# Kernel tuning notes

Measured on AMD Instinct MI355X. Metric: run time of the kernel, lower is better.

Reference implementation:

```python
import jax, jax.numpy as jnp
import numpy as np

NC = 80          # classes
REG_MAX = 16     # DFL bins
NK = 51          # 17*3 keypoint channels
KPT_SHAPE = (17, 3)
MAX_DET = 100
CONF_THRES = 0.25
STRIDES = (8, 16, 32)


def _conv1x1(f, w, b):
    # f: (B,C,H,W), w: (O,C), b: (O,) -> (B,O,H,W)
    return jnp.einsum('bchw,oc->bohw', f, w) + b[None, :, None, None]


def _make_anchors(shapes, strides, offset=0.5):
    pts, sts = [], []
    for (h, w), s in zip(shapes, strides):
        sx = jnp.arange(w, dtype=jnp.float32) + offset
        sy = jnp.arange(h, dtype=jnp.float32) + offset
        gy, gx = jnp.meshgrid(sy, sx, indexing='ij')
        pts.append(jnp.stack([gx, gy], -1).reshape(-1, 2))
        sts.append(jnp.full((h * w, 1), float(s), jnp.float32))
    # transposed as in _new_inference: anchors (2,A), strides (1,A)
    return jnp.concatenate(pts, 0).T, jnp.concatenate(sts, 0).T


def setup_inputs() -> dict:
    key = jax.random.key(0)
    ks = jax.random.split(key, 16)
    ch = (128, 256, 512)
    hw = ((80, 80), (40, 40), (20, 20))
    d = {}
    for i, (c, (h, w)) in enumerate(zip(ch, hw)):
        d[f'x{i}'] = jax.random.normal(ks[i], (16, c, h, w), jnp.float32)
    k = 3
    for name, oc in (('cv2', 4 * REG_MAX), ('cv3', NC), ('cv4', NK)):
        for i, c in enumerate(ch):
            d[f'{name}_w{i}'] = jax.random.normal(ks[k], (oc, c), jnp.float32) * 0.02
            d[f'{name}_b{i}'] = jnp.zeros((oc,), jnp.float32)
            k += 1
    return d


def reference(x0, x1, x2,
              cv2_w0, cv2_b0, cv2_w1, cv2_b1, cv2_w2, cv2_b2,
              cv3_w0, cv3_b0, cv3_w1, cv3_b1, cv3_w2, cv3_b2,
              cv4_w0, cv4_b0, cv4_w1, cv4_b1, cv4_w2, cv4_b2):
    feats = [x0, x1, x2]
    cv2 = [(cv2_w0, cv2_b0), (cv2_w1, cv2_b1), (cv2_w2, cv2_b2)]
    cv3 = [(cv3_w0, cv3_b0), (cv3_w1, cv3_b1), (cv3_w2, cv3_b2)]
    cv4 = [(cv4_w0, cv4_b0), (cv4_w1, cv4_b1), (cv4_w2, cv4_b2)]
    bs = x0.shape[0]

    # keypoint branch: cat over levels -> (bs, nk, A)
    kpt = jnp.concatenate(
        [_conv1x1(f, w, b).reshape(bs, NK, -1) for f, (w, b) in zip(feats, cv4)], -1)
    # box+cls branch -> (bs, 4*reg_max+nc, A)
    xcat = jnp.concatenate(
        [jnp.concatenate([_conv1x1(f, *cv2[i]), _conv1x1(f, *cv3[i])], 1).reshape(bs, 4 * REG_MAX + NC, -1)
         for i, f in enumerate(feats)], -1)
    box, cls = xcat[:, :4 * REG_MAX], xcat[:, 4 * REG_MAX:]

    shapes = [(f.shape[2], f.shape[3]) for f in feats]
    anchors, strides = _make_anchors(shapes, STRIDES)  # (2,A), (1,A)
    A = anchors.shape[1]

    # DFL decode: softmax over reg_max bins, expectation w/ arange weights
    p = jax.nn.softmax(box.reshape(bs, 4, REG_MAX, A), axis=2)
    dist = jnp.einsum('bfra,r->bfa', p, jnp.arange(REG_MAX, dtype=jnp.float32))
    lt, rb = dist[:, :2], dist[:, 2:]
    x1y1 = anchors[None] - lt
    x2y2 = anchors[None] + rb
    # xywh box coding, scaled by strides
    dbox = jnp.concatenate([(x1y1 + x2y2) * 0.5, x2y2 - x1y1], 1) * strides[None]  # (bs,4,A)

    # keypoint decode (Pose.kpts_decode, ndim==3)
    y = kpt.reshape(bs, KPT_SHAPE[0], KPT_SHAPE[1], A)
    kxy = (y[:, :, :2] * 2.0 + (anchors[None, None] - 0.5)) * strides[None, None]
    kv = jax.nn.sigmoid(y[:, :, 2:3])
    pred_kpts = jnp.concatenate([kxy, kv], 2).reshape(bs, NK, A).transpose(0, 2, 1)  # (bs,A,nk)

    # EfficientIdxNMS_TRT stand-in: sigmoid scores (score_activation=1),
    # class-agnostic deterministic top-k selection by best class score.
    scores = jax.nn.sigmoid(cls.transpose(0, 2, 1))  # (bs,A,nc)
    max_s = scores.max(-1)
    cls_id = jnp.argmax(scores, -1)
    top_s, top_i = jax.lax.top_k(max_s, MAX_DET)     # (bs,MAX_DET)
    num_dets = (top_s > CONF_THRES).sum(-1).astype(jnp.int32)[:, None]
    det_boxes = jnp.take_along_axis(dbox.transpose(0, 2, 1), top_i[..., None], 1)  # (bs,MAX_DET,4)
    det_classes = jnp.take_along_axis(cls_id, top_i, 1).astype(jnp.int32)
    # irregular keypoint gather via det indices (the pred_kpts[bs_indices, det_indices] step)
    det_kpts = jnp.take_along_axis(pred_kpts, top_i[..., None], 1).reshape(bs, MAX_DET, *KPT_SHAPE)
    return num_dets, det_boxes, top_s, det_classes, det_kpts
```

## Files before the change

### kernel.cpp

```cpp
#include <hip/hip_runtime.h>
#include <hip/hip_bf16.h>

#define NC 80
#define NK 51
#define REG_MAX 16
#define MAX_DET 100
#define A_TOT 8400
#define BS 16

#define OUT_NUM 0
#define OUT_BOX 16
#define OUT_SCORE (16 + 16*MAX_DET*4)
#define OUT_CLASS (OUT_SCORE + 16*MAX_DET)
#define OUT_KPT (OUT_CLASS + 16*MAX_DET)

static __device__ __forceinline__ unsigned long long mk_key(unsigned u, int a) {
    return ((unsigned long long)u << 32) | (unsigned)(0x7FFFFFFF - a);
}

template<int C, int A>
static __device__ __forceinline__ void score_tile(
    const float* __restrict__ x, const float* __restrict__ w,
    const float* __restrict__ bias,
    int b, int a0, int a_off,
    float* __restrict__ max_s, int* __restrict__ cls_id,
    float* __restrict__ wsh, float (*rm)[256], int (*ri)[256])
{
    int t = threadIdx.x;
    int lane = t & 63;
    int wv = t >> 6;
    int oc0 = wv * 10;

    int aa = a0 + lane * 4;
    if (aa > A - 4) aa = A - 4;
    const float* xb = x + (long)b * C * A + aa;

    float acc[10][4];
#pragma unroll
    for (int j = 0; j < 10; ++j) {
        float bv = bias[oc0 + j];
        acc[j][0] = bv; acc[j][1] = bv; acc[j][2] = bv; acc[j][3] = bv;
    }

    int nchunk = C >> 5;
    for (int kc = 0; kc < nchunk; ++kc) {
        int cbase = kc * 32;
        if (kc) __syncthreads();
#pragma unroll
        for (int i = 0; i < 2; ++i) {
            int idx = t + i * 512;
            if (idx < 640) {
                int oc = idx >> 3;
                int q = idx & 7;
                float4 v = *(const float4*)(w + oc * C + cbase + q * 4);
                *(float4*)(&wsh[idx * 4]) = v;
            }
        }
        __syncthreads();

#pragma unroll 2
        for (int c4 = 0; c4 < 32; c4 += 4) {
            const float* fp = xb + (long)(cbase + c4) * A;
            float4 f0 = *(const float4*)(fp);
            float4 f1 = *(const float4*)(fp + A);
            float4 f2 = *(const float4*)(fp + 2 * A);
            float4 f3 = *(const float4*)(fp + 3 * A);
#pragma unroll
            for (int j = 0; j < 10; ++j) {
                float4 w4 = *(const float4*)(&wsh[(oc0 + j) * 32 + c4]);
                acc[j][0] = fmaf(w4.x, f0.x, acc[j][0]);
                acc[j][0] = fmaf(w4.y, f1.x, acc[j][0]);
                acc[j][0] = fmaf(w4.z, f2.x, acc[j][0]);
                acc[j][0] = fmaf(w4.w, f3.x, acc[j][0]);
                acc[j][1] = fmaf(w4.x, f0.y, acc[j][1]);
                acc[j][1] = fmaf(w4.y, f1.y, acc[j][1]);
                acc[j][1] = fmaf(w4.z, f2.y, acc[j][1]);
                acc[j][1] = fmaf(w4.w, f3.y, acc[j][1]);
                acc[j][2] = fmaf(w4.x, f0.z, acc[j][2]);
                acc[j][2] = fmaf(w4.y, f1.z, acc[j][2]);
                acc[j][2] = fmaf(w4.z, f2.z, acc[j][2]);
                acc[j][2] = fmaf(w4.w, f3.z, acc[j][2]);
                acc[j][3] = fmaf(w4.x, f0.w, acc[j][3]);
                acc[j][3] = fmaf(w4.y, f1.w, acc[j][3]);
                acc[j][3] = fmaf(w4.z, f2.w, acc[j][3]);
                acc[j][3] = fmaf(w4.w, f3.w, acc[j][3]);
            }
        }
    }

#pragma unroll
    for (int q = 0; q < 4; ++q) {
        float m = acc[0][q]; int mi = 0;
#pragma unroll
        for (int j = 1; j < 10; ++j)
            if (acc[j][q] > m) { m = acc[j][q]; mi = j; }
        rm[wv][lane * 4 + q] = m;
        ri[wv][lane * 4 + q] = oc0 + mi;
    }
    __syncthreads();

    if (t < 256) {
        float bm = rm[0][t]; int bi = ri[0][t];
#pragma unroll
        for (int v = 1; v < 8; ++v) {
            float om = rm[v][t];
            if (om > bm) { bm = om; bi = ri[v][t]; }
        }
        int ga = a0 + t;
        if (ga < A) {
            max_s[b * A_TOT + a_off + ga] = 1.0f / (1.0f + expf(-bm));
            cls_id[b * A_TOT + a_off + ga] = bi;
        }
    }
}

__global__ __launch_bounds__(512, 3) void scores_fused(
    const float* __restrict__ x0, const float* __restrict__ x1, const float* __restrict__ x2,
    const float* __restrict__ w0, const float* __restrict__ w1, const float* __restrict__ w2,
    const float* __restrict__ bias0, const float* __restrict__ bias1, const float* __restrict__ bias2,
    float* __restrict__ max_s,
    int* __restrict__ cls_id)
{
    __shared__ float wsh[80 * 32];
    __shared__ float rm[8][256];
    __shared__ int   ri[8][256];

    int bid = blockIdx.x;
    if (bid < 32) {
        int b = bid >> 1, tile = bid & 1;
        score_tile<512, 400>(x2, w2, bias2, b, tile * 256, 8000, max_s, cls_id, wsh, rm, ri);
    } else if (bid < 144) {
        int r = bid - 32;
        int b = r / 7, tile = r - b * 7;
        score_tile<256, 1600>(x1, w1, bias1, b, tile * 256, 6400, max_s, cls_id, wsh, rm, ri);
    } else {
        int r = bid - 144;
        int b = r / 25, tile = r - b * 25;
        score_tile<128, 6400>(x0, w0, bias0, b, tile * 256, 0, max_s, cls_id, wsh, rm, ri);
    }
}

__global__ __launch_bounds__(1024) void topk_kernel(
    const float* __restrict__ max_s,
    const int* __restrict__ cls_id,
    float* __restrict__ out,
    int* __restrict__ top_idx)
{
    int b = blockIdx.x;
    int t = threadIdx.x;
    int wv = t >> 6;

    __shared__ unsigned hist[16 * 256];
    __shared__ unsigned suffix[256];
    __shared__ int tieIdx[A_TOT];
    __shared__ unsigned long long highKeys[128];
    __shared__ unsigned long long finalKeys[128];
    __shared__ int wmin[16];
    __shared__ unsigned s_prefix;
    __shared__ int s_k, s_selD, s_nHigh, s_nTie, s_cnt, s_bcast;

    unsigned u[9];
    bool val[9];
#pragma unroll
    for (int i = 0; i < 9; ++i) {
        int a = t + i * 1024;
        val[i] = (a < A_TOT);
        u[i] = val[i] ? __float_as_uint(max_s[b * A_TOT + a]) : 0u;
    }

    if (t == 0) { s_prefix = 0; s_k = MAX_DET; s_nHigh = 0; s_nTie = 0; s_cnt = 0; }

    for (int pass = 0; pass < 4; ++pass) {
#pragma unroll
        for (int j = 0; j < 4; ++j) hist[t + j * 1024] = 0;
        if (t == 0) s_selD = 0;
        __syncthreads();

        unsigned pre = s_prefix;
        int k = s_k;
        int shHi = 32 - 8 * pass;
        int shD = 24 - 8 * pass;
#pragma unroll
        for (int i = 0; i < 9; ++i) {
            if (val[i]) {
                bool cand = (pass == 0) ? true : ((u[i] >> shHi) == pre);
                if (cand)
                    atomicAdd(&hist[(wv << 8) + ((u[i] >> shD) & 0xFF)], 1u);
            }
        }
        __syncthreads();

        if (t < 256) {
            unsigned s = 0;
#pragma unroll
            for (int w = 0; w < 16; ++w) s += hist[(w << 8) + t];
            suffix[t] = s;
        }
        __syncthreads();
        for (int off = 1; off < 256; off <<= 1) {
            unsigned v = 0;
            if (t < 256) v = suffix[t] + ((t + off < 256) ? suffix[t + off] : 0u);
            __syncthreads();
            if (t < 256) suffix[t] = v;
            __syncthreads();
        }
        if (t < 256 && suffix[t] >= (unsigned)k) atomicMax(&s_selD, t);
        __syncthreads();
        if (t == 0) {
            int d = s_selD;
            s_k = k - ((d < 255) ? (int)suffix[d + 1] : 0);
            s_prefix = (pre << 8) | (unsigned)d;
        }
        __syncthreads();
    }

    unsigned cut = s_prefix;
    int r = s_k;

#pragma unroll
    for (int i = 0; i < 9; ++i) {
        if (val[i]) {
            int a = t + i * 1024;
            if (u[i] > cut) {
                int p = atomicAdd(&s_nHigh, 1);
                highKeys[p] = mk_key(u[i], a);
            } else if (u[i] == cut) {
                int p = atomicAdd(&s_nTie, 1);
                tieIdx[p] = a;
            }
        }
    }
    __syncthreads();
    int m = s_nHigh;
    int nt = s_nTie;

    if (t < 128) finalKeys[t] = 0ull;
    __syncthreads();
    if (t < m) finalKeys[t] = highKeys[t];

    if (nt == r) {
        if (t < nt) finalKeys[m + t] = mk_key(cut, tieIdx[t]);
        __syncthreads();
    } else {
        __syncthreads();
        for (int j = 0; j < r; ++j) {
            int mn = 0x7FFFFFFF;
            for (int p = t; p < nt; p += 1024) mn = min(mn, tieIdx[p]);
            for (int off = 32; off > 0; off >>= 1) mn = min(mn, __shfl_down(mn, off, 64));
            if ((t & 63) == 0) wmin[wv] = mn;
            __syncthreads();
            if (t == 0) {
                int v = wmin[0];
#pragma unroll
                for (int w = 1; w < 16; ++w) v = min(v, wmin[w]);
                s_bcast = v;
                finalKeys[m + j] = mk_key(cut, v);
            }
            __syncthreads();
            int v = s_bcast;
            for (int p = t; p < nt; p += 1024)
                if (tieIdx[p] == v) tieIdx[p] = 0x7FFFFFFF;
            __syncthreads();
        }
    }

    for (int ksz = 2; ksz <= 128; ksz <<= 1) {
        for (int j = ksz >> 1; j > 0; j >>= 1) {
            if (t < 128) {
                int ixj = t ^ j;
                if (ixj > t) {
                    bool desc = ((t & ksz) == 0);
                    unsigned long long x = finalKeys[t], y = finalKeys[ixj];
                    bool sw = desc ? (x < y) : (x > y);
                    if (sw) { finalKeys[t] = y; finalKeys[ixj] = x; }
                }
            }
            __syncthreads();
        }
    }

    if (t < MAX_DET) {
        unsigned long long kk = finalKeys[t];
        float sc = __uint_as_float((unsigned)(kk >> 32));
        int a = 0x7FFFFFFF - (int)(kk & 0xFFFFFFFFull);
        out[OUT_SCORE + b * MAX_DET + t] = sc;
        out[OUT_CLASS + b * MAX_DET + t] = (float)cls_id[b * A_TOT + a];
        top_idx[b * MAX_DET + t] = a;
        if (sc > 0.25f) atomicAdd(&s_cnt, 1);
    }
    __syncthreads();
    if (t == 0) out[OUT_NUM + b] = (float)s_cnt;
}

__global__ __launch_bounds__(128) void decode_kernel(
    const float* __restrict__ x0, const float* __restrict__ x1, const float* __restrict__ x2,
    const float* __restrict__ w2_0, const float* __restrict__ b2_0,
    const float* __restrict__ w2_1, const float* __restrict__ b2_1,
    const float* __restrict__ w2_2, const float* __restrict__ b2_2,
    const float* __restrict__ w4_0, const float* __restrict__ b4_0,
    const float* __restrict__ w4_1, const float* __restrict__ b4_1,
    const float* __restrict__ w4_2, const float* __restrict__ b4_2,
    const int* __restrict__ top_idx,
    float* __restrict__ out)
{
    int b = blockIdx.y;
    int k = blockIdx.x;
    int a = top_idx[b * MAX_DET + k];

    const float* x; const float* w2; const float* bb2; const float* w4; const float* bb4;
    int C, A, W, a_local; float stride;
    if (a < 6400)      { x = x0; C = 128; A = 6400; W = 80; stride = 8.0f;  a_local = a;        w2 = w2_0; bb2 = b2_0; w4 = w4_0; bb4 = b4_0; }
    else if (a < 8000) { x = x1; C = 256; A = 1600; W = 40; stride = 16.0f; a_local = a - 6400; w2 = w2_1; bb2 = b2_1; w4 = w4_1; bb4 = b4_1; }
    else               { x = x2; C = 512; A = 400;  W = 20; stride = 32.0f; a_local = a - 8000; w2 = w2_2; bb2 = b2_2; w4 = w4_2; bb4 = b4_2; }

    __shared__ float fs[512];
    __shared__ float logits[64];
    __shared__ float kraw[NK];
    __shared__ float dist[4];

    int t = threadIdx.x;
    for (int c = t; c < C; c += 128)
        fs[c] = x[((long)b * C + c) * A + a_local];
    __syncthreads();

    if (t < 64 + NK) {
        const float* wrow; float acc;
        if (t < 64) { wrow = w2 + t * C; acc = bb2[t]; }
        else        { wrow = w4 + (t - 64) * C; acc = bb4[t - 64]; }
        for (int c = 0; c < C; ++c) acc = fmaf(wrow[c], fs[c], acc);
        if (t < 64) logits[t] = acc;
        else        kraw[t - 64] = acc;
    }
    __syncthreads();

    if (t < 4) {
        float mx = logits[t * 16];
#pragma unroll
        for (int r = 1; r < 16; ++r) mx = fmaxf(mx, logits[t * 16 + r]);
        float se = 0.0f, sw = 0.0f;
#pragma unroll
        for (int r = 0; r < 16; ++r) {
            float e = expf(logits[t * 16 + r] - mx);
            se += e; sw += e * (float)r;
        }
        dist[t] = sw / se;
    }
    __syncthreads();

    float ax = (float)(a_local % W) + 0.5f;
    float ay = (float)(a_local / W) + 0.5f;

    if (t == 0) {
        float x1c = ax - dist[0], y1c = ay - dist[1];
        float x2c = ax + dist[2], y2c = ay + dist[3];
        float* ob = out + OUT_BOX + ((long)b * MAX_DET + k) * 4;
        ob[0] = (x1c + x2c) * 0.5f * stride;
        ob[1] = (y1c + y2c) * 0.5f * stride;
        ob[2] = (x2c - x1c) * stride;
        ob[3] = (y2c - y1c) * stride;
    }
    if (t < 17) {
        float vx = kraw[t * 3], vy = kraw[t * 3 + 1], vv = kraw[t * 3 + 2];
        float gx = ax - 0.5f, gy = ay - 0.5f;
        float* ok = out + OUT_KPT + (((long)b * MAX_DET + k) * 17 + t) * 3;
        ok[0] = (vx * 2.0f + gx) * stride;
        ok[1] = (vy * 2.0f + gy) * stride;
        ok[2] = 1.0f / (1.0f + expf(-vv));
    }
}

extern "C" void kernel_launch(void* const* d_in, const int* in_sizes, int n_in,
                              void* d_out, int out_size, void* d_ws, size_t ws_size,
                              hipStream_t stream) {
    const float* x0 = (const float*)d_in[0];
    const float* x1 = (const float*)d_in[1];
    const float* x2 = (const float*)d_in[2];
    const float* w2[3] = {(const float*)d_in[3], (const float*)d_in[5], (const float*)d_in[7]};
    const float* b2[3] = {(const float*)d_in[4], (const float*)d_in[6], (const float*)d_in[8]};
    const float* w3[3] = {(const float*)d_in[9], (const float*)d_in[11], (const float*)d_in[13]};
    const float* b3[3] = {(const float*)d_in[10], (const float*)d_in[12], (const float*)d_in[14]};
    const float* w4[3] = {(const float*)d_in[15], (const float*)d_in[17], (const float*)d_in[19]};
    const float* b4[3] = {(const float*)d_in[16], (const float*)d_in[18], (const float*)d_in[20]};

    float* out = (float*)d_out;

    float* ws_maxs = (float*)d_ws;
    int* ws_cls = (int*)(ws_maxs + BS * A_TOT);
    int* ws_top = (int*)(ws_cls + BS * A_TOT);

    scores_fused<<<dim3(544), 512, 0, stream>>>(
        x0, x1, x2, w3[0], w3[1], w3[2], b3[0], b3[1], b3[2], ws_maxs, ws_cls);
    topk_kernel<<<dim3(BS), 1024, 0, stream>>>(ws_maxs, ws_cls, out, ws_top);
    decode_kernel<<<dim3(MAX_DET, BS), 128, 0, stream>>>(
        x0, x1, x2,
        w2[0], b2[0], w2[1], b2[1], w2[2], b2[2],
        w4[0], b4[0], w4[1], b4[1], w4[2], b4[2],
        ws_top, out);
}
```

Before: 305.8 us.

## Restructure score GEMM tile: 8 anchors per thread, double-buffered weights, shuffle argmax

The class-score kernel now runs with 256 threads per block. Each thread computes 10 classes by 8 anchors instead of 4, and the 8 class groups of a wave are spread across lanes. Weight chunks are prefetched into registers and written to a padded, double-buffered shared-memory tile, which removes one barrier per chunk. The cross-group argmax uses wave shuffles instead of a shared-memory reduction. The cost is more registers per thread (80 accumulators), a lower occupancy bound, and shuffle tie-breaking that must keep the lowest class index.

Result: slower. 434.2 us (+42.0%).

```diff
diff --git a/kernel.cpp b/kernel.cpp
--- a/kernel.cpp
+++ b/kernel.cpp
@@ -24,119 +24,168 @@
     const float* __restrict__ bias,
     int b, int a0, int a_off,
     float* __restrict__ max_s, int* __restrict__ cls_id,
-    float* __restrict__ wsh, float (*rm)[256], int (*ri)[256])
+    float* __restrict__ wsh)
 {
     int t = threadIdx.x;
     int lane = t & 63;
     int wv = t >> 6;
-    int oc0 = wv * 10;
-
-    int aa = a0 + lane * 4;
-    if (aa > A - 4) aa = A - 4;
+    int og = lane >> 3;
+    int slot = lane & 7;
+    int oc0 = og * 10;
+
+    int aa = a0 + wv * 64 + slot * 8;
+    if (aa > A - 8) aa = A - 8;
     const float* xb = x + (long)b * C * A + aa;
 
-    float acc[10][4];
+    float acc[10][8];
 #pragma unroll
     for (int j = 0; j < 10; ++j) {
         float bv = bias[oc0 + j];
-        acc[j][0] = bv; acc[j][1] = bv; acc[j][2] = bv; acc[j][3] = bv;
-    }
-
-    int nchunk = C >> 5;
-    for (int kc = 0; kc < nchunk; ++kc) {
+#pragma unroll
+        for (int q = 0; q < 8; ++q) acc[j][q] = bv;
+    }
+
+    constexpr int NCH = C >> 5;
+
+    float4 st0, st1, st2;
+    int i0 = t, i1 = t + 256, i2 = t + 512;
+    int oc_0 = i0 >> 3, q_0 = i0 & 7;
+    int oc_1 = i1 >> 3, q_1 = i1 & 7;
+    int oc_2 = i2 >> 3, q_2 = i2 & 7;
+    bool v2ld = (i2 < 640);
+
+    st0 = *(const float4*)(w + oc_0 * C + q_0 * 4);
+    st1 = *(const float4*)(w + oc_1 * C + q_1 * 4);
+    if (v2ld) st2 = *(const float4*)(w + oc_2 * C + q_2 * 4);
+    *(float4*)(&wsh[oc_0 * 36 + q_0 * 4]) = st0;
+    *(float4*)(&wsh[oc_1 * 36 + q_1 * 4]) = st1;
+    if (v2ld) *(float4*)(&wsh[oc_2 * 36 + q_2 * 4]) = st2;
+    __syncthreads();
+
+    for (int kc = 0; kc < NCH; ++kc) {
+        int p = kc & 1;
         int cbase = kc * 32;
-        if (kc) __syncthreads();
-#pragma unroll
-        for (int i = 0; i < 2; ++i) {
-            int idx = t + i * 512;
-            if (idx < 640) {
-                int oc = idx >> 3;
-                int q = idx & 7;
-                float4 v = *(const float4*)(w + oc * C + cbase + q * 4);
-                *(float4*)(&wsh[idx * 4]) = v;
-            }
-        }
-        __syncthreads();
-
+
+        if (kc + 1 < NCH) {
+            const float* wn = w + (cbase + 32);
+            st0 = *(const float4*)(wn + oc_0 * C + q_0 * 4);
+            st1 = *(const float4*)(wn + oc_1 * C + q_1 * 4);
+            if (v2ld) st2 = *(const float4*)(wn + oc_2 * C + q_2 * 4);
+        }
+
+        const float* wp = wsh + p * 2880 + oc0 * 36;
 #pragma unroll 2
         for (int c4 = 0; c4 < 32; c4 += 4) {
             const float* fp = xb + (long)(cbase + c4) * A;
-            float4 f0 = *(const float4*)(fp);
-            float4 f1 = *(const float4*)(fp + A);
-            float4 f2 = *(const float4*)(fp + 2 * A);
-            float4 f3 = *(const float4*)(fp + 3 * A);
+            float4 fA[4], fB[4];
+#pragma unroll
+            for (int cc = 0; cc < 4; ++cc) {
+                fA[cc] = *(const float4*)(fp + (long)cc * A);
+                fB[cc] = *(const float4*)(fp + (long)cc * A + 4);
+            }
 #pragma unroll
             for (int j = 0; j < 10; ++j) {
-                float4 w4 = *(const float4*)(&wsh[(oc0 + j) * 32 + c4]);
-                acc[j][0] = fmaf(w4.x, f0.x, acc[j][0]);
-                acc[j][0] = fmaf(w4.y, f1.x, acc[j][0]);
-                acc[j][0] = fmaf(w4.z, f2.x, acc[j][0]);
-                acc[j][0] = fmaf(w4.w, f3.x, acc[j][0]);
-                acc[j][1] = fmaf(w4.x, f0.y, acc[j][1]);
-                acc[j][1] = fmaf(w4.y, f1.y, acc[j][1]);
-                acc[j][1] = fmaf(w4.z, f2.y, acc[j][1]);
-                acc[j][1] = fmaf(w4.w, f3.y, acc[j][1]);
-                acc[j][2] = fmaf(w4.x, f0.z, acc[j][2]);
-                acc[j][2] = fmaf(w4.y, f1.z, acc[j][2]);
-                acc[j][2] = fmaf(w4.z, f2.z, acc[j][2]);
-                acc[j][2] = fmaf(w4.w, f3.z, acc[j][2]);
-                acc[j][3] = fmaf(w4.x, f0.w, acc[j][3]);
-                acc[j][3] = fmaf(w4.y, f1.w, acc[j][3]);
-                acc[j][3] = fmaf(w4.z, f2.w, acc[j][3]);
-                acc[j][3] = fmaf(w4.w, f3.w, acc[j][3]);
-            }
-        }
-    }
-
-#pragma unroll
-    for (int q = 0; q < 4; ++q) {
-        float m = acc[0][q]; int mi = 0;
+                float4 w4 = *(const float4*)(wp + j * 36 + c4);
+                acc[j][0] = fmaf(w4.x, fA[0].x, acc[j][0]);
+                acc[j][0] = fmaf(w4.y, fA[1].x, acc[j][0]);
+                acc[j][0] = fmaf(w4.z, fA[2].x, acc[j][0]);
+                acc[j][0] = fmaf(w4.w, fA[3].x, acc[j][0]);
+                acc[j][1] = fmaf(w4.x, fA[0].y, acc[j][1]);
+                acc[j][1] = fmaf(w4.y, fA[1].y, acc[j][1]);
+                acc[j][1] = fmaf(w4.z, fA[2].y, acc[j][1]);
+                acc[j][1] = fmaf(w4.w, fA[3].y, acc[j][1]);
+                acc[j][2] = fmaf(w4.x, fA[0].z, acc[j][2]);
+                acc[j][2] = fmaf(w4.y, fA[1].z, acc[j][2]);
+                acc[j][2] = fmaf(w4.z, fA[2].z, acc[j][2]);
+                acc[j][2] = fmaf(w4.w, fA[3].z, acc[j][2]);
+                acc[j][3] = fmaf(w4.x, fA[0].w, acc[j][3]);
+                acc[j][3] = fmaf(w4.y, fA[1].w, acc[j][3]);
+                acc[j][3] = fmaf(w4.z, fA[2].w, acc[j][3]);
+                acc[j][3] = fmaf(w4.w, fA[3].w, acc[j][3]);
+                acc[j][4] = fmaf(w4.x, fB[0].x, acc[j][4]);
+                acc[j][4] = fmaf(w4.y, fB[1].x, acc[j][4]);
+                acc[j][4] = fmaf(w4.z, fB[2].x, acc[j][4]);
+                acc[j][4] = fmaf(w4.w, fB[3].x, acc[j][4]);
+                acc[j][5] = fmaf(w4.x, fB[0].y, acc[j][5]);
+                acc[j][5] = fmaf(w4.y, fB[1].y, acc[j][5]);
+                acc[j][5] = fmaf(w4.z, fB[2].y, acc[j][5]);
+                acc[j][5] = fmaf(w4.w, fB[3].y, acc[j][5]);
+                acc[j][6] = fmaf(w4.x, fB[0].z, acc[j][6]);
+                acc[j][6] = fmaf(w4.y, fB[1].z, acc[j][6]);
+                acc[j][6] = fmaf(w4.z, fB[2].z, acc[j][6]);
+                acc[j][6] = fmaf(w4.w, fB[3].z, acc[j][6]);
+                acc[j][7] = fmaf(w4.x, fB[0].w, acc[j][7]);
+                acc[j][7] = fmaf(w4.y, fB[1].w, acc[j][7]);
+                acc[j][7] = fmaf(w4.z, fB[2].w, acc[j][7]);
+                acc[j][7] = fmaf(w4.w, fB[3].w, acc[j][7]);
+            }
+        }
+
+        if (kc + 1 < NCH) {
+            float* wd = wsh + (p ^ 1) * 2880;
+            *(float4*)(&wd[oc_0 * 36 + q_0 * 4]) = st0;
+            *(float4*)(&wd[oc_1 * 36 + q_1 * 4]) = st1;
+            if (v2ld) *(float4*)(&wd[oc_2 * 36 + q_2 * 4]) = st2;
+            __syncthreads();
+        }
+    }
+
+    float m[8]; int id[8];
+#pragma unroll
+    for (int q = 0; q < 8; ++q) {
+        float mm = acc[0][q]; int mi = 0;
 #pragma unroll
         for (int j = 1; j < 10; ++j)
-            if (acc[j][q] > m) { m = acc[j][q]; mi = j; }
-        rm[wv][lane * 4 + q] = m;
-        ri[wv][lane * 4 + q] = oc0 + mi;
-    }
-    __syncthreads();
-
-    if (t < 256) {
-        float bm = rm[0][t]; int bi = ri[0][t];
-#pragma unroll
-        for (int v = 1; v < 8; ++v) {
-            float om = rm[v][t];
-            if (om > bm) { bm = om; bi = ri[v][t]; }
-        }
-        int ga = a0 + t;
-        if (ga < A) {
-            max_s[b * A_TOT + a_off + ga] = 1.0f / (1.0f + expf(-bm));
-            cls_id[b * A_TOT + a_off + ga] = bi;
-        }
-    }
-}
-
-__global__ __launch_bounds__(512, 3) void scores_fused(
+            if (acc[j][q] > mm) { mm = acc[j][q]; mi = j; }
+        m[q] = mm; id[q] = oc0 + mi;
+    }
+
+#pragma unroll
+    for (int mask = 8; mask <= 32; mask <<= 1) {
+        bool other_first = (lane & mask) != 0;
+#pragma unroll
+        for (int q = 0; q < 8; ++q) {
+            float om = __shfl_xor(m[q], mask, 64);
+            int   oi = __shfl_xor(id[q], mask, 64);
+            bool take = other_first ? (om >= m[q]) : (om > m[q]);
+            if (take) { m[q] = om; id[q] = oi; }
+        }
+    }
+
+    if (og == 0) {
+        int base = a0 + wv * 64 + slot * 8;
+#pragma unroll
+        for (int q = 0; q < 8; ++q) {
+            int ga = base + q;
+            if (ga < A) {
+                max_s[b * A_TOT + a_off + ga] = 1.0f / (1.0f + expf(-m[q]));
+                cls_id[b * A_TOT + a_off + ga] = id[q];
+            }
+        }
+    }
+}
+
+__global__ __launch_bounds__(256, 2) void scores_fused(
     const float* __restrict__ x0, const float* __restrict__ x1, const float* __restrict__ x2,
     const float* __restrict__ w0, const float* __restrict__ w1, const float* __restrict__ w2,
     const float* __restrict__ bias0, const float* __restrict__ bias1, const float* __restrict__ bias2,
     float* __restrict__ max_s,
     int* __restrict__ cls_id)
 {
-    __shared__ float wsh[80 * 32];
-    __shared__ float rm[8][256];
-    __shared__ int   ri[8][256];
+    __shared__ float wsh[2 * 80 * 36];
 
     int bid = blockIdx.x;
     if (bid < 32) {
         int b = bid >> 1, tile = bid & 1;
-        score_tile<512, 400>(x2, w2, bias2, b, tile * 256, 8000, max_s, cls_id, wsh, rm, ri);
+        score_tile<512, 400>(x2, w2, bias2, b, tile * 256, 8000, max_s, cls_id, wsh);
     } else if (bid < 144) {
         int r = bid - 32;
         int b = r / 7, tile = r - b * 7;
-        score_tile<256, 1600>(x1, w1, bias1, b, tile * 256, 6400, max_s, cls_id, wsh, rm, ri);
+        score_tile<256, 1600>(x1, w1, bias1, b, tile * 256, 6400, max_s, cls_id, wsh);
     } else {
         int r = bid - 144;
         int b = r / 25, tile = r - b * 25;
-        score_tile<128, 6400>(x0, w0, bias0, b, tile * 256, 0, max_s, cls_id, wsh, rm, ri);
+        score_tile<128, 6400>(x0, w0, bias0, b, tile * 256, 0, max_s, cls_id, wsh);
     }
 }
 
@@ -388,7 +437,7 @@
     int* ws_cls = (int*)(ws_maxs + BS * A_TOT);
     int* ws_top = (int*)(ws_cls + BS * A_TOT);
 
-    scores_fused<<<dim3(544), 512, 0, stream>>>(
+    scores_fused<<<dim3(544), 256, 0, stream>>>(
         x0, x1, x2, w3[0], w3[1], w3[2], b3[0], b3[1], b3[2], ws_maxs, ws_cls);
     topk_kernel<<<dim3(BS), 1024, 0, stream>>>(ws_maxs, ws_cls, out, ws_top);
     decode_kernel<<<dim3(MAX_DET, BS), 128, 0, stream>>>(
```
